# Kernel tuning notes

Hardware: AMD Instinct MI355X
Metric: run time of the kernel (lower is better)

## Reference

```python
import jax, jax.numpy as jnp
import numpy as np

B, N, C = 4, 2048, 768
H = 12
D = C // H  # head_dim = 64


def setup_inputs() -> dict:
    key = jax.random.key(0)
    k1, k2, k3, k4, k5 = jax.random.split(key, 5)
    s = 0.02
    return {
        "x": jax.random.normal(k1, (B, N, C), dtype=jnp.float32),
        "qkv_w": jax.random.normal(k2, (3 * C, C), dtype=jnp.float32) * s,
        "qkv_b": jax.random.normal(k3, (3 * C,), dtype=jnp.float32) * s,
        "proj_w": jax.random.normal(k4, (C, C), dtype=jnp.float32) * s,
        "proj_b": jax.random.normal(k5, (C,), dtype=jnp.float32) * s,
    }


def reference(x, qkv_w, qkv_b, proj_w, proj_b):
    b, n, c = x.shape
    # qkv projection (torch Linear: x @ W.T + b) -> [B,N,3,H,D] -> [3,B,H,N,D]
    qkv = (x @ qkv_w.T + qkv_b).reshape(b, n, 3, H, D).transpose(2, 0, 3, 1, 4)
    q, k, v = qkv[0], qkv[1], qkv[2]
    scale = D ** (-0.5)
    attn = jnp.einsum("bhqd,bhkd->bhqk", q, k) * scale
    attn = jax.nn.softmax(attn, axis=-1)
    # dropout is identity in eval mode
    out = jnp.einsum("bhqk,bhkd->bhqd", attn, v)  # [B,H,N,D]
    out = out.transpose(0, 2, 1, 3).reshape(b, n, c)
    return out @ proj_w.T + proj_b
```

## Files before the change

kernel.cpp:

```cpp
#include <hip/hip_runtime.h>
#include <hip/hip_bf16.h>
#include <stdint.h>

typedef __bf16 bf16_t;
typedef __bf16 bf16x8 __attribute__((ext_vector_type(8)));
typedef float f32x4 __attribute__((ext_vector_type(4)));
typedef unsigned int u32x4 __attribute__((ext_vector_type(4)));

#define NB 4
#define NH 12
#define ND 64
#define NN 2048
#define NC 768

__device__ __forceinline__ void async_copy16(const bf16_t* g, bf16_t* l) {
    __builtin_amdgcn_global_load_lds((__attribute__((address_space(1))) void*)(void*)g,
                                     (__attribute__((address_space(3))) void*)l, 16, 0, 0);
}

__device__ __forceinline__ unsigned pack_bf2(float a, float b) {
    union { bf16_t e[2]; unsigned u; } t;
    t.e[0] = (bf16_t)a;
    t.e[1] = (bf16_t)b;
    return t.u;
}

__global__ void cast3_kernel(const float* __restrict__ s0, bf16_t* __restrict__ d0, int n0,
                             const float* __restrict__ s1, bf16_t* __restrict__ d1, int n1,
                             const float* __restrict__ s2, bf16_t* __restrict__ d2, int n2) {
    int i = blockIdx.x * blockDim.x + threadIdx.x;
    const float* s;
    bf16_t* d;
    int j;
    if (i < n0)           { s = s0; d = d0; j = i; }
    else if (i < n0 + n1) { s = s1; d = d1; j = i - n0; }
    else if (i < n0 + n1 + n2) { s = s2; d = d2; j = i - n0 - n1; }
    else return;
    float4 v = ((const float4*)s)[j];
    union { bf16_t e[4]; uint2 u; } t;
    t.e[0] = (bf16_t)v.x; t.e[1] = (bf16_t)v.y; t.e[2] = (bf16_t)v.z; t.e[3] = (bf16_t)v.w;
    ((uint2*)d)[j] = t.u;
}

__device__ __forceinline__ int vperm(int s) {
    return (s & 32) | (((s >> 2) & 3) << 3) | (((s >> 4) & 1) << 2) | (s & 3);
}


__launch_bounds__(256)
__global__ void qkv_gemm_kernel(const bf16_t* __restrict__ X, const bf16_t* __restrict__ W,
                                const float* __restrict__ bias,
                                bf16_t* __restrict__ Q, bf16_t* __restrict__ K, bf16_t* __restrict__ V)
{
    __shared__ __align__(16) bf16_t sA[128 * 64];
    __shared__ __align__(16) bf16_t sB[128 * 64];
    const int tid  = threadIdx.x;
    const int lane = tid & 63;
    const int w    = tid >> 6;
    const int wm   = w & 1, wn = w >> 1;
    const int wg  = blockIdx.y * 64 + blockIdx.x;
    const int xcd = wg & 7;
    const int idx = wg >> 3;
    const int m0  = ((xcd >> 1) * 16 + idx / 9) * 128;
    const int n0  = ((xcd & 1) * 9 + idx % 9) * 128;
    const int lrow = lane & 15;
    const int quad = lane >> 4;
    const int arow = lane >> 3;
    const int gch  = (lane & 7) ^ arow;

    f32x4 zero = {0.f, 0.f, 0.f, 0.f};
    f32x4 acc[4][4];
#pragma unroll
    for (int i = 0; i < 4; ++i)
#pragma unroll
        for (int j = 0; j < 4; ++j) acc[i][j] = zero;

    for (int kt = 0; kt < NC; kt += 64) {
        __syncthreads();
        for (int c = w; c < 16; c += 4) {
            async_copy16(X + (size_t)(m0 + c * 8 + arow) * NC + kt + gch * 8, sA + c * 512);
            async_copy16(W + (size_t)(n0 + c * 8 + arow) * NC + kt + gch * 8, sB + c * 512);
        }
        __syncthreads();
#pragma unroll
        for (int hh = 0; hh < 2; ++hh) {
            bf16x8 af[4], bfr[4];
#pragma unroll
            for (int i = 0; i < 4; ++i) {
                int r = wm * 64 + i * 16 + lrow;
                af[i] = *(const bf16x8*)(sA + r * 64 + (((hh * 4 + quad) ^ (r & 7)) * 8));
            }
#pragma unroll
            for (int j = 0; j < 4; ++j) {
                int r = wn * 64 + j * 16 + lrow;
                bfr[j] = *(const bf16x8*)(sB + r * 64 + (((hh * 4 + quad) ^ (r & 7)) * 8));
            }
#pragma unroll
            for (int i = 0; i < 4; ++i)
#pragma unroll
                for (int j = 0; j < 4; ++j)
                    acc[i][j] = __builtin_amdgcn_mfma_f32_16x16x32_bf16(af[i], bfr[j], acc[i][j], 0, 0, 0);
        }
    }

    const int colbase = n0 + wn * 64;
    const int t3 = colbase / NC;
    const int h  = (colbase % NC) / ND;
    const float qscale = 0.125f * 1.44269504088896340736f;

#pragma unroll
    for (int j = 0; j < 4; ++j) {
        const int d  = j * 16 + lrow;
        const float bv = bias[colbase + d];
#pragma unroll
        for (int i = 0; i < 4; ++i) {
            const int rowg = m0 + wm * 64 + i * 16 + quad * 4;
            const int bb = rowg >> 11;
            const int nn = rowg & 2047;
            if (t3 == 2) {
                union { bf16_t e[4]; uint2 u; } pk;
#pragma unroll
                for (int p = 0; p < 4; ++p) pk.e[p] = (bf16_t)(acc[i][j][p] + bv);
                const int pos = (nn & ~63) | vperm(nn & 63);
                *(uint2*)(V + ((size_t)(bb * NH + h) * ND + d) * NN + pos) = pk.u;
            } else {
                bf16_t* outb = t3 ? K : Q;
#pragma unroll
                for (int p = 0; p < 4; ++p) {
                    float val = acc[i][j][p] + bv;
                    if (t3 == 0) val *= qscale;
                    outb[((size_t)(bb * NH + h) * NN + nn + p) * ND + d] = (bf16_t)val;
                }
            }
        }
    }
}

#define WAIT_BAR(N)                                              \
    asm volatile("s_waitcnt vmcnt(" #N ")" ::: "memory");        \
    __builtin_amdgcn_sched_barrier(0);                           \
    __builtin_amdgcn_s_barrier();                                \
    __builtin_amdgcn_sched_barrier(0);

#define STAGE(BUF)                                               \
    {                                                            \
        async_copy16(kp, sK[BUF] + w * 512);                     \
        async_copy16(vp, sV[BUF] + w * 512);                     \
        kp += (size_t)64 * ND; vp += 64;                         \
    }

#define ATTN_COMPUTE(CUR)                                                                            \
    {                                                                                                \
        const bf16_t* sKh = sK[CUR];                                                                 \
        const bf16_t* sVh = sV[CUR];                                                                 \
        f32x4 s[4];                                                                                  \
        __builtin_amdgcn_s_setprio(1);                                                               \
        _Pragma("unroll")                                                                            \
        for (int blk = 0; blk < 4; ++blk) {                                                          \
            bf16x8 a0 = *(const bf16x8*)(sKh + off[blk][0]);                                         \
            bf16x8 a1 = *(const bf16x8*)(sKh + off[blk][1]);                                         \
            f32x4 z = zero;                                                                          \
            z = __builtin_amdgcn_mfma_f32_16x16x32_bf16(a0, qb0, z, 0, 0, 0);                        \
            z = __builtin_amdgcn_mfma_f32_16x16x32_bf16(a1, qb1, z, 0, 0, 0);                        \
            s[blk] = z;                                                                              \
        }                                                                                            \
        __builtin_amdgcn_s_setprio(0);                                                               \
        u32x4 pu0 = {0, 0, 0, 0}, pu1 = {0, 0, 0, 0};                                                \
        _Pragma("unroll")                                                                            \
        for (int blk = 0; blk < 4; ++blk) {                                                          \
            float e0 = __builtin_amdgcn_exp2f(s[blk][0]);                                            \
            float e1 = __builtin_amdgcn_exp2f(s[blk][1]);                                            \
            float e2 = __builtin_amdgcn_exp2f(s[blk][2]);                                            \
            float e3 = __builtin_amdgcn_exp2f(s[blk][3]);                                            \
            unsigned lo = pack_bf2(e0, e1), hi = pack_bf2(e2, e3);                                   \
            if (blk == 0)      { pu0[0] = lo; pu0[1] = hi; }                                         \
            else if (blk == 1) { pu0[2] = lo; pu0[3] = hi; }                                         \
            else if (blk == 2) { pu1[0] = lo; pu1[1] = hi; }                                         \
            else               { pu1[2] = lo; pu1[3] = hi; }                                         \
        }                                                                                            \
        bf16x8 pe0 = __builtin_bit_cast(bf16x8, pu0);                                                \
        bf16x8 pe1 = __builtin_bit_cast(bf16x8, pu1);                                                \
        __builtin_amdgcn_s_setprio(1);                                                               \
        lacc = __builtin_amdgcn_mfma_f32_16x16x32_bf16(ones, pe0, lacc, 0, 0, 0);                    \
        lacc = __builtin_amdgcn_mfma_f32_16x16x32_bf16(ones, pe1, lacc, 0, 0, 0);                    \
        _Pragma("unroll")                                                                            \
        for (int db = 0; db < 4; ++db) {                                                             \
            bf16x8 v0 = *(const bf16x8*)(sVh + off[db][0]);                                          \
            bf16x8 v1 = *(const bf16x8*)(sVh + off[db][1]);                                          \
            o[db] = __builtin_amdgcn_mfma_f32_16x16x32_bf16(v0, pe0, o[db], 0, 0, 0);                \
            o[db] = __builtin_amdgcn_mfma_f32_16x16x32_bf16(v1, pe1, o[db], 0, 0, 0);                \
        }                                                                                            \
        __builtin_amdgcn_s_setprio(0);                                                               \
    }

__launch_bounds__(512, 6)
__global__ void attn_kernel(const bf16_t* __restrict__ Q, const bf16_t* __restrict__ K,
                            const bf16_t* __restrict__ Vt, bf16_t* __restrict__ O)
{
    __shared__ __align__(16) bf16_t sK[3][64 * 64];
    __shared__ __align__(16) bf16_t sV[3][64 * 64];
    bf16_t* sQ = sK[0];
    const int tid  = threadIdx.x;
    const int lane = tid & 63;
    const int w    = tid >> 6;
    const int qt   = blockIdx.x;
    const int h    = blockIdx.y;
    const int b    = blockIdx.z;
    const int lrow = lane & 15;
    const int quad = lane >> 4;
    const int arow = lane >> 3;
    const int gch  = (lane & 7) ^ arow;
    const size_t head_off = (size_t)(b * NH + h) * NN * ND;
    const bf16_t* qh = Q  + head_off;
    const bf16_t* kh = K  + head_off;
    const bf16_t* vh = Vt + head_off;

#pragma unroll
    for (int c = 0; c < 2; ++c)
        async_copy16(qh + (size_t)(qt * 128 + (w * 2 + c) * 8 + arow) * ND + gch * 8,
                     sQ + (w * 2 + c) * 512);
    __syncthreads();

    bf16x8 qb0, qb1;
    {
        int r = w * 16 + lrow;
        qb0 = *(const bf16x8*)(sQ + r * 64 + (((0 * 4 + quad) ^ (r & 7)) * 8));
        qb1 = *(const bf16x8*)(sQ + r * 64 + (((1 * 4 + quad) ^ (r & 7)) * 8));
    }
    __syncthreads();

    bf16x8 ones;
#pragma unroll
    for (int p = 0; p < 8; ++p) ones[p] = (bf16_t)1.0f;

    int off[4][2];
#pragma unroll
    for (int blk = 0; blk < 4; ++blk) {
        int r = blk * 16 + lrow;
        off[blk][0] = r * 64 + ((quad ^ (r & 7)) * 8);
        off[blk][1] = r * 64 + (((4 + quad) ^ (r & 7)) * 8);
    }

    f32x4 zero = {0.f, 0.f, 0.f, 0.f};
    f32x4 o[4];
#pragma unroll
    for (int db = 0; db < 4; ++db) o[db] = zero;
    f32x4 lacc = zero;

    const bf16_t* kp = kh + (size_t)(w * 8 + arow) * ND + gch * 8;
    const bf16_t* vp = vh + (size_t)(w * 8 + arow) * NN + gch * 8;

    STAGE(0);
    STAGE(1);
    WAIT_BAR(2);

    int cur = 0;
    for (int it = 0; it < NN / 64 - 2; ++it) {
        int nxt = cur + 2; if (nxt >= 3) nxt -= 3;
        STAGE(nxt);
        ATTN_COMPUTE(cur);
        WAIT_BAR(2);
        cur = (cur + 1 == 3) ? 0 : cur + 1;
    }
    ATTN_COMPUTE(cur);
    WAIT_BAR(0);
    cur = (cur + 1 == 3) ? 0 : cur + 1;
    ATTN_COMPUTE(cur);

    {
        const float rl = 1.0f / lacc[0];
        const int n = qt * 128 + w * 16 + lrow;
        const size_t rowoff = ((size_t)(b * NN + n)) * NC + h * ND;
#pragma unroll
        for (int db = 0; db < 4; ++db) {
            union { bf16_t e[4]; uint2 u; } pk;
#pragma unroll
            for (int p = 0; p < 4; ++p) pk.e[p] = (bf16_t)(o[db][p] * rl);
            *(uint2*)(O + rowoff + db * 16 + quad * 4) = pk.u;
        }
    }
}

__launch_bounds__(256)
__global__ void proj_gemm_kernel(const bf16_t* __restrict__ A, const bf16_t* __restrict__ W,
                                 const float* __restrict__ bias, float* __restrict__ out)
{
    __shared__ __align__(16) bf16_t sA[128 * 64];
    __shared__ __align__(16) bf16_t sB[128 * 64];
    const int tid  = threadIdx.x;
    const int lane = tid & 63;
    const int w    = tid >> 6;
    const int wm   = w & 1, wn = w >> 1;
    const int wg  = blockIdx.y * 64 + blockIdx.x;
    const int xcd = wg & 7;
    const int idx = wg >> 3;
    const int m0  = (xcd * 8 + idx / 6) * 128;
    const int n0  = (idx % 6) * 128;
    const int lrow = lane & 15;
    const int quad = lane >> 4;
    const int arow = lane >> 3;
    const int gch  = (lane & 7) ^ arow;

    f32x4 zero = {0.f, 0.f, 0.f, 0.f};
    f32x4 acc[4][4];
#pragma unroll
    for (int i = 0; i < 4; ++i)
#pragma unroll
        for (int j = 0; j < 4; ++j) acc[i][j] = zero;

    for (int kt = 0; kt < NC; kt += 64) {
        __syncthreads();
        for (int c = w; c < 16; c += 4) {
            async_copy16(A + (size_t)(m0 + c * 8 + arow) * NC + kt + gch * 8, sA + c * 512);
            async_copy16(W + (size_t)(n0 + c * 8 + arow) * NC + kt + gch * 8, sB + c * 512);
        }
        __syncthreads();
#pragma unroll
        for (int hh = 0; hh < 2; ++hh) {
            bf16x8 af[4], bfr[4];
#pragma unroll
            for (int i = 0; i < 4; ++i) {
                int r = wm * 64 + i * 16 + lrow;
                af[i] = *(const bf16x8*)(sA + r * 64 + (((hh * 4 + quad) ^ (r & 7)) * 8));
            }
#pragma unroll
            for (int j = 0; j < 4; ++j) {
                int r = wn * 64 + j * 16 + lrow;
                bfr[j] = *(const bf16x8*)(sB + r * 64 + (((hh * 4 + quad) ^ (r & 7)) * 8));
            }
#pragma unroll
            for (int i = 0; i < 4; ++i)
#pragma unroll
                for (int j = 0; j < 4; ++j)
                    acc[i][j] = __builtin_amdgcn_mfma_f32_16x16x32_bf16(af[i], bfr[j], acc[i][j], 0, 0, 0);
        }
    }

#pragma unroll
    for (int j = 0; j < 4; ++j) {
        const int colg = n0 + wn * 64 + j * 16 + lrow;
        const float bv = bias[colg];
#pragma unroll
        for (int i = 0; i < 4; ++i) {
            const int rowg = m0 + wm * 64 + i * 16 + quad * 4;
#pragma unroll
            for (int p = 0; p < 4; ++p)
                out[(size_t)(rowg + p) * NC + colg] = acc[i][j][p] + bv;
        }
    }
}

extern "C" void kernel_launch(void* const* d_in, const int* in_sizes, int n_in,
                              void* d_out, int out_size, void* d_ws, size_t ws_size,
                              hipStream_t stream) {
    const float* x      = (const float*)d_in[0];
    const float* qkv_w  = (const float*)d_in[1];
    const float* qkv_b  = (const float*)d_in[2];
    const float* proj_w = (const float*)d_in[3];
    const float* proj_b = (const float*)d_in[4];
    float* out = (float*)d_out;

    char* ws = (char*)d_ws;
    bf16_t* xb    = (bf16_t*)ws; ws += (size_t)8192 * 768 * 2;
    bf16_t* wqkv  = (bf16_t*)ws; ws += (size_t)2304 * 768 * 2;
    bf16_t* wproj = (bf16_t*)ws; ws += (size_t)768 * 768 * 2;
    bf16_t* qb    = (bf16_t*)ws; ws += (size_t)NB * NH * NN * ND * 2;
    bf16_t* kb    = (bf16_t*)ws; ws += (size_t)NB * NH * NN * ND * 2;
    bf16_t* vb    = (bf16_t*)ws; ws += (size_t)NB * NH * NN * ND * 2;
    bf16_t* ab    = (bf16_t*)ws; ws += (size_t)8192 * 768 * 2;

    const int c0 = 8192 * 768 / 4, c1 = 2304 * 768 / 4, c2 = 768 * 768 / 4;
    cast3_kernel<<<(c0 + c1 + c2 + 255) / 256, 256, 0, stream>>>(x, xb, c0, qkv_w, wqkv, c1, proj_w, wproj, c2);

    qkv_gemm_kernel<<<dim3(8192 / 128, 2304 / 128), 256, 0, stream>>>(xb, wqkv, qkv_b, qb, kb, vb);
    attn_kernel<<<dim3(NN / 128, NH, NB), 512, 0, stream>>>(qb, kb, vb, ab);
    proj_gemm_kernel<<<dim3(8192 / 128, 768 / 128), 256, 0, stream>>>(ab, wproj, proj_b, out);
}
```

Baseline: 204.4 us.

## Software-pipeline QK^T and PV across tiles, halve proj GEMM M tile

```diff
diff --git a/kernel.cpp b/kernel.cpp
--- a/kernel.cpp
+++ b/kernel.cpp
@@ -149,29 +149,32 @@
         kp += (size_t)64 * ND; vp += 64;                         \
     }
 
-#define ATTN_COMPUTE(CUR)                                                                            \
+#define S_STEP(SOUT, KB)                                                                  \
+    {                                                                                     \
+        const bf16_t* sKh = (KB);                                                         \
+        __builtin_amdgcn_s_setprio(1);                                                    \
+        _Pragma("unroll")                                                                 \
+        for (int blk = 0; blk < 4; ++blk) {                                               \
+            bf16x8 a0 = *(const bf16x8*)(sKh + off[blk][0]);                              \
+            bf16x8 a1 = *(const bf16x8*)(sKh + off[blk][1]);                              \
+            f32x4 z = zero;                                                               \
+            z = __builtin_amdgcn_mfma_f32_16x16x32_bf16(a0, qb0, z, 0, 0, 0);             \
+            z = __builtin_amdgcn_mfma_f32_16x16x32_bf16(a1, qb1, z, 0, 0, 0);             \
+            SOUT[blk] = z;                                                                \
+        }                                                                                 \
+        __builtin_amdgcn_s_setprio(0);                                                    \
+    }
+
+#define FINISH_STEP(SIN, VB)                                                                         \
     {                                                                                                \
-        const bf16_t* sKh = sK[CUR];                                                                 \
-        const bf16_t* sVh = sV[CUR];                                                                 \
-        f32x4 s[4];                                                                                  \
-        __builtin_amdgcn_s_setprio(1);                                                               \
-        _Pragma("unroll")                                                                            \
-        for (int blk = 0; blk < 4; ++blk) {                                                          \
-            bf16x8 a0 = *(const bf16x8*)(sKh + off[blk][0]);                                         \
-            bf16x8 a1 = *(const bf16x8*)(sKh + off[blk][1]);                                         \
-            f32x4 z = zero;                                                                          \
-            z = __builtin_amdgcn_mfma_f32_16x16x32_bf16(a0, qb0, z, 0, 0, 0);                        \
-            z = __builtin_amdgcn_mfma_f32_16x16x32_bf16(a1, qb1, z, 0, 0, 0);                        \
-            s[blk] = z;                                                                              \
-        }                                                                                            \
-        __builtin_amdgcn_s_setprio(0);                                                               \
+        const bf16_t* sVh = (VB);                                                                    \
         u32x4 pu0 = {0, 0, 0, 0}, pu1 = {0, 0, 0, 0};                                                \
         _Pragma("unroll")                                                                            \
         for (int blk = 0; blk < 4; ++blk) {                                                          \
-            float e0 = __builtin_amdgcn_exp2f(s[blk][0]);                                            \
-            float e1 = __builtin_amdgcn_exp2f(s[blk][1]);                                            \
-            float e2 = __builtin_amdgcn_exp2f(s[blk][2]);                                            \
-            float e3 = __builtin_amdgcn_exp2f(s[blk][3]);                                            \
+            float e0 = __builtin_amdgcn_exp2f(SIN[blk][0]);                                          \
+            float e1 = __builtin_amdgcn_exp2f(SIN[blk][1]);                                          \
+            float e2 = __builtin_amdgcn_exp2f(SIN[blk][2]);                                          \
+            float e3 = __builtin_amdgcn_exp2f(SIN[blk][3]);                                          \
             unsigned lo = pack_bf2(e0, e1), hi = pack_bf2(e2, e3);                                   \
             if (blk == 0)      { pu0[0] = lo; pu0[1] = hi; }                                         \
             else if (blk == 1) { pu0[2] = lo; pu0[3] = hi; }                                         \
@@ -254,18 +257,26 @@
     STAGE(1);
     WAIT_BAR(2);
 
-    int cur = 0;
-    for (int it = 0; it < NN / 64 - 2; ++it) {
-        int nxt = cur + 2; if (nxt >= 3) nxt -= 3;
-        STAGE(nxt);
-        ATTN_COMPUTE(cur);
-        WAIT_BAR(2);
-        cur = (cur + 1 == 3) ? 0 : cur + 1;
-    }
-    ATTN_COMPUTE(cur);
+    f32x4 sXA[4], sXB[4];
+    S_STEP(sXA, sK[0]);
+
+    int c0 = 0, c1 = 1, c2 = 2;
+    for (int it = 0; it < NN / 64 - 2; it += 2) {
+        WAIT_BAR(0);
+        STAGE(c2);
+        S_STEP(sXB, sK[c1]);
+        FINISH_STEP(sXA, sV[c0]);
+        { int t = c0; c0 = c1; c1 = c2; c2 = t; }
+        WAIT_BAR(0);
+        STAGE(c2);
+        S_STEP(sXA, sK[c1]);
+        FINISH_STEP(sXB, sV[c0]);
+        { int t = c0; c0 = c1; c1 = c2; c2 = t; }
+    }
     WAIT_BAR(0);
-    cur = (cur + 1 == 3) ? 0 : cur + 1;
-    ATTN_COMPUTE(cur);
+    S_STEP(sXB, sK[c1]);
+    FINISH_STEP(sXA, sV[c0]);
+    FINISH_STEP(sXB, sV[c1]);
 
     {
         const float rl = 1.0f / lacc[0];
@@ -285,16 +296,16 @@
 __global__ void proj_gemm_kernel(const bf16_t* __restrict__ A, const bf16_t* __restrict__ W,
                                  const float* __restrict__ bias, float* __restrict__ out)
 {
-    __shared__ __align__(16) bf16_t sA[128 * 64];
+    __shared__ __align__(16) bf16_t sA[64 * 64];
     __shared__ __align__(16) bf16_t sB[128 * 64];
     const int tid  = threadIdx.x;
     const int lane = tid & 63;
     const int w    = tid >> 6;
     const int wm   = w & 1, wn = w >> 1;
-    const int wg  = blockIdx.y * 64 + blockIdx.x;
+    const int wg  = blockIdx.y * 128 + blockIdx.x;
     const int xcd = wg & 7;
     const int idx = wg >> 3;
-    const int m0  = (xcd * 8 + idx / 6) * 128;
+    const int m0  = (xcd * 16 + idx / 6) * 64;
     const int n0  = (idx % 6) * 128;
     const int lrow = lane & 15;
     const int quad = lane >> 4;
@@ -302,25 +313,28 @@
     const int gch  = (lane & 7) ^ arow;
 
     f32x4 zero = {0.f, 0.f, 0.f, 0.f};
-    f32x4 acc[4][4];
-#pragma unroll
-    for (int i = 0; i < 4; ++i)
+    f32x4 acc[2][4];
+#pragma unroll
+    for (int i = 0; i < 2; ++i)
 #pragma unroll
         for (int j = 0; j < 4; ++j) acc[i][j] = zero;
 
     for (int kt = 0; kt < NC; kt += 64) {
         __syncthreads();
-        for (int c = w; c < 16; c += 4) {
-            async_copy16(A + (size_t)(m0 + c * 8 + arow) * NC + kt + gch * 8, sA + c * 512);
-            async_copy16(W + (size_t)(n0 + c * 8 + arow) * NC + kt + gch * 8, sB + c * 512);
+        for (int c = w; c < 24; c += 4) {
+            if (c < 8)
+                async_copy16(A + (size_t)(m0 + c * 8 + arow) * NC + kt + gch * 8, sA + c * 512);
+            else
+                async_copy16(W + (size_t)(n0 + (c - 8) * 8 + arow) * NC + kt + gch * 8,
+                             sB + (c - 8) * 512);
         }
         __syncthreads();
 #pragma unroll
         for (int hh = 0; hh < 2; ++hh) {
-            bf16x8 af[4], bfr[4];
-#pragma unroll
-            for (int i = 0; i < 4; ++i) {
-                int r = wm * 64 + i * 16 + lrow;
+            bf16x8 af[2], bfr[4];
+#pragma unroll
+            for (int i = 0; i < 2; ++i) {
+                int r = wm * 32 + i * 16 + lrow;
                 af[i] = *(const bf16x8*)(sA + r * 64 + (((hh * 4 + quad) ^ (r & 7)) * 8));
             }
 #pragma unroll
@@ -329,7 +343,7 @@
                 bfr[j] = *(const bf16x8*)(sB + r * 64 + (((hh * 4 + quad) ^ (r & 7)) * 8));
             }
 #pragma unroll
-            for (int i = 0; i < 4; ++i)
+            for (int i = 0; i < 2; ++i)
 #pragma unroll
                 for (int j = 0; j < 4; ++j)
                     acc[i][j] = __builtin_amdgcn_mfma_f32_16x16x32_bf16(af[i], bfr[j], acc[i][j], 0, 0, 0);
@@ -341,8 +355,8 @@
         const int colg = n0 + wn * 64 + j * 16 + lrow;
         const float bv = bias[colg];
 #pragma unroll
-        for (int i = 0; i < 4; ++i) {
-            const int rowg = m0 + wm * 64 + i * 16 + quad * 4;
+        for (int i = 0; i < 2; ++i) {
+            const int rowg = m0 + wm * 32 + i * 16 + quad * 4;
 #pragma unroll
             for (int p = 0; p < 4; ++p)
                 out[(size_t)(rowg + p) * NC + colg] = acc[i][j][p] + bv;
@@ -374,5 +388,5 @@
 
     qkv_gemm_kernel<<<dim3(8192 / 128, 2304 / 128), 256, 0, stream>>>(xb, wqkv, qkv_b, qb, kb, vb);
     attn_kernel<<<dim3(NN / 128, NH, NB), 512, 0, stream>>>(qb, kb, vb, ab);
-    proj_gemm_kernel<<<dim3(8192 / 128, 768 / 128), 256, 0, stream>>>(ab, wproj, proj_b, out);
-}
+    proj_gemm_kernel<<<dim3(8192 / 64, 768 / 128), 256, 0, stream>>>(ab, wproj, proj_b, out);
+}
```

Result: slower. 221.7 us (+8.5%).
